# Kernel tuning notes

Hardware: AMD Instinct MI355X
Metric: run time of the kernel (lower is better)

The kernel has to match this reference:

```python
import jax, jax.numpy as jnp
import numpy as np

Q_MIN = 0.01
PT_THLD = 0.9
MAX_ETA = 4.0
LW_REP = 1.0
LW_NOISE = 0.1
LW_COWARD = 0.1
EPS = 1e-9

N_HITS = 50000
N_CLUSTERS = 1024  # cluster id 0 = noise, ids 1..K-1 = objects
D_EMB = 32


def setup_inputs() -> dict:
    key = jax.random.key(0)
    k0, k1, k2, k3, k4, k5 = jax.random.split(key, 6)
    beta = jax.random.uniform(k0, (N_HITS,), dtype=jnp.float32)
    x = jax.random.normal(k1, (N_HITS, D_EMB), dtype=jnp.float32)
    pt = jax.random.uniform(k2, (N_HITS,), dtype=jnp.float32)
    eta = jax.random.normal(k3, (N_HITS,), dtype=jnp.float32)
    reconstructable = jax.random.randint(k4, (N_HITS,), 0, 2, dtype=jnp.int32)
    cluster_ids = jax.random.randint(k5, (N_HITS,), 0, N_CLUSTERS, dtype=jnp.int64)
    return {
        'beta': beta, 'x': x, 'pt': pt, 'eta': eta,
        'reconstructable': reconstructable, 'cluster_ids': cluster_ids,
        'n_clusters': N_CLUSTERS,
    }


def reference(beta, x, pt, eta, reconstructable, cluster_ids, n_clusters):
    K = int(n_clusters)
    n_hits = beta.shape[0]
    n_part = K - 1  # objects of interest (excluding noise id 0)

    # charge q_j = arctanh(beta)^2 + q_min
    q = jnp.arctanh(jnp.clip(beta, 0.0, 1.0 - 1e-4)) ** 2 + Q_MIN  # [N]

    # attractive membership mask [N, K-1]: hit j belongs to object k and passes filters
    oids = jnp.arange(1, K)
    hit_ok = (reconstructable > 0) & (pt > PT_THLD) & (jnp.abs(eta) < MAX_ETA)
    att = (cluster_ids[:, None] == oids[None, :]) & hit_ok[:, None]
    attf = att.astype(q.dtype)

    # condensation point per object: hit with max charge within the object
    alphas = jnp.argmax(q[:, None] * attf, axis=0)  # [K-1]
    q_k = q[alphas]
    x_k = x[alphas]  # [K-1, D]

    # pairwise Euclidean distances, GEMM form (avoids [N,K,D] intermediate)
    d2 = (jnp.sum(x * x, axis=1)[:, None]
          + jnp.sum(x_k * x_k, axis=1)[None, :]
          - 2.0 * (x @ x_k.T))
    dist = jnp.sqrt(jnp.maximum(d2, 1e-12))  # [N, K-1]

    qw = q[:, None] * q_k[None, :]

    n_hits_oi = jnp.sum(hit_ok).astype(q.dtype)
    norm_att = EPS + n_hits_oi - n_part
    norm_rep = EPS + (n_part - 1) * n_hits

    v_att = jnp.sum(qw * (dist ** 2) * attf) / norm_att

    rep = (~att) & (dist < 1.0)  # max_n_rep=0 -> no subsampling
    v_rep = jnp.sum(qw * (1.0 - dist) * rep.astype(q.dtype)) / norm_rep

    l_coward = jnp.mean(1.0 - beta[alphas])

    noise_mask = (cluster_ids <= 0).astype(q.dtype)  # noise_threshold = 0
    l_noise = jnp.sum(beta * noise_mask) / jnp.maximum(jnp.sum(noise_mask), 1.0)

    total = v_att + LW_REP * v_rep + LW_NOISE * l_noise + LW_COWARD * l_coward
    return total
```

## Files before the change

kernel.cpp:

```cpp
#include <hip/hip_runtime.h>
#include <math.h>

namespace {

constexpr int D = 32;
constexpr int KOBJ = 1023;
constexpr float QMIN = 0.01f;
constexpr float PTT = 0.9f;
constexpr float METAETA = 4.0f;

typedef __attribute__((ext_vector_type(8))) short short8;
typedef __attribute__((ext_vector_type(4))) float f32x4;

__device__ inline float waveSum(float v) {
#pragma unroll
  for (int o = 32; o > 0; o >>= 1) v += __shfl_down(v, o, 64);
  return v;
}

__device__ inline ushort f2bf(float f) {
  unsigned u = __float_as_uint(f);
  return (ushort)((u + 0x7FFFu + ((u >> 16) & 1u)) >> 16);
}

__global__ void k_init(float* acc, int* flagNZ, unsigned long long* keys,
                       const int* __restrict__ cidw, int N) {
  int i = blockIdx.x * blockDim.x + threadIdx.x;
  if (i < KOBJ) keys[i] = 0ull;
  if (i < 8) acc[i] = 0.f;
  if (blockIdx.x == 0) {
    if (threadIdx.x == 0) flagNZ[0] = 0;
    __syncthreads();
    for (int jj = threadIdx.x; jj < 1024; jj += blockDim.x) {
      int idx = 2 * jj + 1;
      if (idx < N && cidw[idx] != 0) flagNZ[0] = 1;
    }
  }
}

__global__ __launch_bounds__(256) void k_hits(
    const float* __restrict__ beta, const float* __restrict__ x,
    const float* __restrict__ pt, const float* __restrict__ eta,
    const int* __restrict__ recon, const int* __restrict__ cidw,
    int N, const int* __restrict__ flagNZ,
    float* acc, unsigned long long* keys,
    float* __restrict__ qArr, float* __restrict__ nxArr,
    int* __restrict__ attkArr) {
  int t = threadIdx.x;
  int j = blockIdx.x * 256 + t;
  int is64 = (flagNZ[0] == 0);
  bool ok = false;
  if (j < N) {
    int cid = is64 ? cidw[2 * j] : cidw[j];
    float b = beta[j];
    float bc = fminf(fmaxf(b, 0.f), 1.f - 1e-4f);
    float tt = atanhf(bc);
    float q = tt * tt + QMIN;
    ok = (recon[j] > 0) && (pt[j] > PTT) && (fabsf(eta[j]) < METAETA);
    float nx = 0.f;
    const float4* xr = (const float4*)(x + (size_t)j * D);
#pragma unroll
    for (int i2 = 0; i2 < 8; ++i2) {
      float4 v = xr[i2];
      nx += v.x * v.x + v.y * v.y + v.z * v.z + v.w * v.w;
    }
    int attk = (ok && cid >= 1) ? cid : 0;
    qArr[j] = q;
    nxArr[j] = nx;
    attkArr[j] = attk;
    if (cid <= 0) {
      atomicAdd(&acc[2], b);
      atomicAdd(&acc[3], 1.f);
    }
    if (attk >= 1) {
      unsigned long long key =
          (((unsigned long long)__float_as_uint(q)) << 32) |
          (unsigned long long)(0xFFFFFFFFu - (unsigned)j);
      atomicMax(&keys[attk - 1], key);
    }
  }
  unsigned long long bal = __ballot(ok);
  if ((t & 63) == 0 && bal)
    atomicAdd(&acc[4], (float)__popcll(bal));
}

__global__ __launch_bounds__(256, 2) void k_clusters(
    const float* __restrict__ beta, const float* __restrict__ x,
    const unsigned long long* __restrict__ keys,
    const float* __restrict__ qArr, const float* __restrict__ nxArr,
    int* __restrict__ alphaArr, float2* __restrict__ qnk,
    ushort* __restrict__ xkbT, float* acc) {
  int k = blockIdx.x * blockDim.x + threadIdx.x;
  float cw = 0.f;
  if (k < KOBJ) {
    unsigned long long key = keys[k];
    int alpha = (key != 0ull) ? (int)(0xFFFFFFFFu - (unsigned)(key & 0xFFFFFFFFull)) : 0;
    alphaArr[k] = alpha;
    qnk[k] = make_float2(qArr[alpha], nxArr[alpha]);
    const float4* s4 = (const float4*)(x + (size_t)alpha * D);
    float4 v[8];
#pragma unroll
    for (int i = 0; i < 8; ++i) v[i] = s4[i];
#pragma unroll
    for (int s = 0; s < 4; ++s) {
      float4 v0 = v[2 * s], v1 = v[2 * s + 1];
      ushort* dst = xkbT + (size_t)s * 8192 + (size_t)k * 8;
      dst[0] = f2bf(v0.x); dst[1] = f2bf(v0.y);
      dst[2] = f2bf(v0.z); dst[3] = f2bf(v0.w);
      dst[4] = f2bf(v1.x); dst[5] = f2bf(v1.y);
      dst[6] = f2bf(v1.z); dst[7] = f2bf(v1.w);
    }
    cw = 1.f - beta[alpha];
  } else if (k == KOBJ) {
    qnk[k] = make_float2(0.f, 1e30f);
#pragma unroll
    for (int s = 0; s < 4; ++s) {
      ushort* dst = xkbT + (size_t)s * 8192 + (size_t)k * 8;
#pragma unroll
      for (int e = 0; e < 8; ++e) dst[e] = 0;
    }
  }
  float s = waveSum(cw);
  if ((threadIdx.x & 63) == 0 && s != 0.f) atomicAdd(&acc[5], s);
}

__global__ __launch_bounds__(256, 4) void k_pair(
    const float* __restrict__ x, int N,
    const float* __restrict__ qArr, const float* __restrict__ nxArr,
    const int* __restrict__ attkArr, const int* __restrict__ alphaArr,
    const float2* __restrict__ qnk, const ushort* __restrict__ xkbT,
    float* acc) {
  __shared__ char lds[16384 + 2048 + 48];
  float* redS = (float*)(lds + 16384 + 2048);
  int t = threadIdx.x;
  int wv = t >> 6;
  int ln = t & 63;
  int ot = blockIdx.y;
  int ob = ot * 256;
  int rowbase = blockIdx.x * 64;

#pragma unroll
  for (int i = 0; i < 4; ++i) {
    int c = wv * 4 + i;
    const char* src = (const char*)xkbT + (c >> 2) * 16384 + ob * 16 + (c & 3) * 1024;
    *(short8*)(lds + c * 1024 + ln * 16) = *(const short8*)(src + ln * 16);
  }
  if (wv < 2) {
    const char* src = (const char*)qnk + ob * 8 + wv * 1024;
    *(short8*)(lds + 16384 + wv * 1024 + ln * 16) = *(const short8*)(src + ln * 16);
  }

  int lr = ln & 15;
  int lk = ln >> 4;
  int wrow = rowbase + wv * 16;

  short8 am2;
  {
    int row = min(wrow + lr, N - 1);
    const float* p = x + (size_t)row * D + lk * 8;
    float4 v0 = *(const float4*)p;
    float4 v1 = *(const float4*)(p + 4);
    am2[0] = (short)f2bf(-2.f * v0.x); am2[1] = (short)f2bf(-2.f * v0.y);
    am2[2] = (short)f2bf(-2.f * v0.z); am2[3] = (short)f2bf(-2.f * v0.w);
    am2[4] = (short)f2bf(-2.f * v1.x); am2[5] = (short)f2bf(-2.f * v1.y);
    am2[6] = (short)f2bf(-2.f * v1.z); am2[7] = (short)f2bf(-2.f * v1.w);
  }
  float nxr[4], qrow[4];
#pragma unroll
  for (int i = 0; i < 4; ++i) {
    int row = wrow + lk * 4 + i;
    int rc = min(row, N - 1);
    nxr[i] = (row < N) ? nxArr[rc] : 1e37f;
    qrow[i] = (row < N) ? qArr[rc] : 0.f;
  }
  __syncthreads();

  const float2* qnkS = (const float2*)(lds + 16384);
  float rep = 0.f;
#pragma unroll
  for (int tt = 0; tt < 16; ++tt) {
    int o = tt * 16 + lr;
    short8 b = *(const short8*)(lds + lk * 4096 + o * 16);
    float2 qn = qnkS[o];
    float nk = qn.y;
    f32x4 c = {nxr[0] + nk, nxr[1] + nk, nxr[2] + nk, nxr[3] + nk};
    f32x4 s = __builtin_amdgcn_mfma_f32_16x16x32_bf16(am2, b, c, 0, 0, 0);
    float m = fminf(fminf(s[0], s[1]), fminf(s[2], s[3]));
    if (__any(m < 1.f)) {
      float qk = qn.x;
#pragma unroll
      for (int i = 0; i < 4; ++i) {
        if (s[i] < 1.f)
          rep += qrow[i] * qk * (1.f - sqrtf(fmaxf(s[i], 1e-12f)));
      }
    }
  }

  float attc = 0.f, repSub = 0.f;
  if (ot == 0) {
    int j = rowbase + (t >> 2);
    int qt = t & 3;
    if (j < N) {
      int attk = attkArr[j];
      if (attk >= 1) {
        int k0 = attk - 1;
        int alpha = alphaArr[k0];
        float2 qn = qnk[k0];
        const float4* xj = (const float4*)(x + (size_t)j * D + qt * 8);
        const float4* xk = (const float4*)(x + (size_t)alpha * D + qt * 8);
        float4 a0 = xj[0], a1 = xj[1], b0 = xk[0], b1 = xk[1];
        float dot = a0.x * b0.x + a0.y * b0.y + a0.z * b0.z + a0.w * b0.w
                  + a1.x * b1.x + a1.y * b1.y + a1.z * b1.z + a1.w * b1.w;
        dot += __shfl_xor(dot, 1, 4);
        dot += __shfl_xor(dot, 2, 4);
        if (qt == 0) {
          float d2 = nxArr[j] + qn.y - 2.f * dot;
          float w = qArr[j] * qn.x;
          attc = w * fmaxf(d2, 1e-12f);
          if (d2 < 1.f)
            repSub = w * (1.f - sqrtf(fmaxf(d2, 1e-12f)));
        }
      }
    }
  }

  float sw = waveSum(rep);
  float sa = waveSum(attc);
  float sr = waveSum(repSub);
  if (ln == 0) {
    redS[wv] = sw;
    redS[4 + wv] = sa;
    redS[8 + wv] = sr;
  }
  __syncthreads();
  if (t == 0) {
    float tot = (redS[0] + redS[1]) + (redS[2] + redS[3]);
    float ta = (redS[4] + redS[5]) + (redS[6] + redS[7]);
    float tr = (redS[8] + redS[9]) + (redS[10] + redS[11]);
    if (tot != tr) atomicAdd(&acc[1], tot - tr);
    if (ta != 0.f) atomicAdd(&acc[0], ta);
  }
}

__global__ void k_final(const float* __restrict__ acc, int N, float* out) {
  if (threadIdx.x == 0 && blockIdx.x == 0) {
    double attSum = acc[0], repSum = acc[1], noiseSum = acc[2];
    double noiseCnt = acc[3], okCnt = acc[4], cowardSum = acc[5];
    double norm_att = 1e-9 + okCnt - (double)KOBJ;
    double norm_rep = 1e-9 + (double)(KOBJ - 1) * (double)N;
    double v_att = attSum / norm_att;
    double v_rep = repSum / norm_rep;
    double l_coward = cowardSum / (double)KOBJ;
    double l_noise = noiseSum / fmax(noiseCnt, 1.0);
    out[0] = (float)(v_att + 1.0 * v_rep + 0.1 * l_noise + 0.1 * l_coward);
  }
}

}

extern "C" void kernel_launch(void* const* d_in, const int* in_sizes, int n_in,
                              void* d_out, int out_size, void* d_ws, size_t ws_size,
                              hipStream_t stream) {
  const float* beta = (const float*)d_in[0];
  const float* x = (const float*)d_in[1];
  const float* pt = (const float*)d_in[2];
  const float* eta = (const float*)d_in[3];
  const int* recon = (const int*)d_in[4];
  const int* cidw = (const int*)d_in[5];
  int N = in_sizes[0];
  float* out = (float*)d_out;

  char* w = (char*)d_ws;
  float* acc = (float*)w;
  int* flagNZ = (int*)(w + 40);
  unsigned long long* keys = (unsigned long long*)(w + 64);
  int* alphaArr = (int*)(w + 8256);
  float2* qnk = (float2*)(w + 12352);
  ushort* xkbT = (ushort*)(w + 20544);
  float* qArr = (float*)(w + 86080);
  float* nxArr = (float*)(w + 86080 + (size_t)N * 4);
  int* attkArr = (int*)(w + 86080 + (size_t)N * 8);

  int nbN = (N + 255) / 256;
  int rowgroups = (N + 63) / 64;

  k_init<<<4, 256, 0, stream>>>(acc, flagNZ, keys, cidw, N);
  k_hits<<<nbN, 256, 0, stream>>>(beta, x, pt, eta, recon, cidw, N, flagNZ,
                                  acc, keys, qArr, nxArr, attkArr);
  k_clusters<<<4, 256, 0, stream>>>(beta, x, keys, qArr, nxArr,
                                    alphaArr, qnk, xkbT, acc);
  dim3 gp(rowgroups, 4);
  k_pair<<<gp, 256, 0, stream>>>(x, N, qArr, nxArr, attkArr,
                                 alphaArr, qnk, xkbT, acc);
  k_final<<<1, 64, 0, stream>>>(acc, N, out);
}
```

Measured before the change: 62.69 us.

## Process two row tiles per wave, load object tile via global_load_lds, branchless repulsion

Each block now covers 128 rows instead of 64. Every wave issues two MFMAs per object tile, so each LDS-staged object tile is reused across twice as many hit rows and half as many blocks restage it. The object tile and charges are copied straight into LDS with global_load_lds instead of going through registers. The __any-guarded repulsion branch becomes a branchless fmaxf(0, 1-sqrt) form, which evaluates sqrt for every pair and trades compute for no divergence; the main loop's unroll is reduced to 4 and the occupancy hint is dropped.

```diff
diff --git a/kernel.cpp b/kernel.cpp
--- a/kernel.cpp
+++ b/kernel.cpp
@@ -11,6 +11,11 @@
 
 typedef __attribute__((ext_vector_type(8))) short short8;
 typedef __attribute__((ext_vector_type(4))) float f32x4;
+
+#define GLOAD_LDS16(g, l)                                              \
+  __builtin_amdgcn_global_load_lds(                                    \
+      (const __attribute__((address_space(1))) void*)(g),              \
+      (__attribute__((address_space(3))) void*)(l), 16, 0, 0)
 
 __device__ inline float waveSum(float v) {
 #pragma unroll
@@ -124,95 +129,99 @@
   if ((threadIdx.x & 63) == 0 && s != 0.f) atomicAdd(&acc[5], s);
 }
 
-__global__ __launch_bounds__(256, 4) void k_pair(
+__global__ __launch_bounds__(256) void k_pair(
     const float* __restrict__ x, int N,
     const float* __restrict__ qArr, const float* __restrict__ nxArr,
     const int* __restrict__ attkArr, const int* __restrict__ alphaArr,
     const float2* __restrict__ qnk, const ushort* __restrict__ xkbT,
     float* acc) {
-  __shared__ char lds[16384 + 2048 + 48];
-  float* redS = (float*)(lds + 16384 + 2048);
+  __shared__ char lds[16384 + 2048 + 64];
+  float* redS = (float*)(lds + 18432);
   int t = threadIdx.x;
   int wv = t >> 6;
   int ln = t & 63;
   int ot = blockIdx.y;
   int ob = ot * 256;
-  int rowbase = blockIdx.x * 64;
-
-#pragma unroll
-  for (int i = 0; i < 4; ++i) {
-    int c = wv * 4 + i;
-    const char* src = (const char*)xkbT + (c >> 2) * 16384 + ob * 16 + (c & 3) * 1024;
-    *(short8*)(lds + c * 1024 + ln * 16) = *(const short8*)(src + ln * 16);
-  }
-  if (wv < 2) {
-    const char* src = (const char*)qnk + ob * 8 + wv * 1024;
-    *(short8*)(lds + 16384 + wv * 1024 + ln * 16) = *(const short8*)(src + ln * 16);
+  int rowbase = blockIdx.x * 128;
+
+  for (int c = wv; c < 18; c += 4) {
+    const char* src;
+    if (c < 16)
+      src = (const char*)xkbT + (c >> 2) * 16384 + ob * 16 + (c & 3) * 1024;
+    else
+      src = (const char*)qnk + ob * 8 + (c - 16) * 1024;
+    GLOAD_LDS16(src + ln * 16, lds + c * 1024);
   }
 
   int lr = ln & 15;
   int lk = ln >> 4;
-  int wrow = rowbase + wv * 16;
-
-  short8 am2;
-  {
-    int row = min(wrow + lr, N - 1);
+  int wrow = rowbase + wv * 32;
+
+  short8 am2[2];
+#pragma unroll
+  for (int rt = 0; rt < 2; ++rt) {
+    int row = min(wrow + rt * 16 + lr, N - 1);
     const float* p = x + (size_t)row * D + lk * 8;
     float4 v0 = *(const float4*)p;
     float4 v1 = *(const float4*)(p + 4);
-    am2[0] = (short)f2bf(-2.f * v0.x); am2[1] = (short)f2bf(-2.f * v0.y);
-    am2[2] = (short)f2bf(-2.f * v0.z); am2[3] = (short)f2bf(-2.f * v0.w);
-    am2[4] = (short)f2bf(-2.f * v1.x); am2[5] = (short)f2bf(-2.f * v1.y);
-    am2[6] = (short)f2bf(-2.f * v1.z); am2[7] = (short)f2bf(-2.f * v1.w);
-  }
-  float nxr[4], qrow[4];
-#pragma unroll
-  for (int i = 0; i < 4; ++i) {
-    int row = wrow + lk * 4 + i;
-    int rc = min(row, N - 1);
-    nxr[i] = (row < N) ? nxArr[rc] : 1e37f;
-    qrow[i] = (row < N) ? qArr[rc] : 0.f;
-  }
+    short8 a;
+    a[0] = (short)f2bf(-2.f * v0.x); a[1] = (short)f2bf(-2.f * v0.y);
+    a[2] = (short)f2bf(-2.f * v0.z); a[3] = (short)f2bf(-2.f * v0.w);
+    a[4] = (short)f2bf(-2.f * v1.x); a[5] = (short)f2bf(-2.f * v1.y);
+    a[6] = (short)f2bf(-2.f * v1.z); a[7] = (short)f2bf(-2.f * v1.w);
+    am2[rt] = a;
+  }
+  float nxr[2][4], qrow[2][4];
+#pragma unroll
+  for (int rt = 0; rt < 2; ++rt)
+#pragma unroll
+    for (int i = 0; i < 4; ++i) {
+      int row = wrow + rt * 16 + lk * 4 + i;
+      int rc = min(row, N - 1);
+      nxr[rt][i] = (row < N) ? nxArr[rc] : 1e37f;
+      qrow[rt][i] = (row < N) ? qArr[rc] : 0.f;
+    }
   __syncthreads();
 
   const float2* qnkS = (const float2*)(lds + 16384);
   float rep = 0.f;
-#pragma unroll
+#pragma unroll 4
   for (int tt = 0; tt < 16; ++tt) {
     int o = tt * 16 + lr;
     short8 b = *(const short8*)(lds + lk * 4096 + o * 16);
     float2 qn = qnkS[o];
     float nk = qn.y;
-    f32x4 c = {nxr[0] + nk, nxr[1] + nk, nxr[2] + nk, nxr[3] + nk};
-    f32x4 s = __builtin_amdgcn_mfma_f32_16x16x32_bf16(am2, b, c, 0, 0, 0);
-    float m = fminf(fminf(s[0], s[1]), fminf(s[2], s[3]));
-    if (__any(m < 1.f)) {
-      float qk = qn.x;
-#pragma unroll
-      for (int i = 0; i < 4; ++i) {
-        if (s[i] < 1.f)
-          rep += qrow[i] * qk * (1.f - sqrtf(fmaxf(s[i], 1e-12f)));
-      }
+    float qk = qn.x;
+    f32x4 c0 = {nxr[0][0] + nk, nxr[0][1] + nk, nxr[0][2] + nk, nxr[0][3] + nk};
+    f32x4 c1 = {nxr[1][0] + nk, nxr[1][1] + nk, nxr[1][2] + nk, nxr[1][3] + nk};
+    f32x4 s0 = __builtin_amdgcn_mfma_f32_16x16x32_bf16(am2[0], b, c0, 0, 0, 0);
+    f32x4 s1 = __builtin_amdgcn_mfma_f32_16x16x32_bf16(am2[1], b, c1, 0, 0, 0);
+#pragma unroll
+    for (int i = 0; i < 4; ++i) {
+      rep += qrow[0][i] * qk * fmaxf(0.f, 1.f - sqrtf(fmaxf(s0[i], 1e-12f)));
+      rep += qrow[1][i] * qk * fmaxf(0.f, 1.f - sqrtf(fmaxf(s1[i], 1e-12f)));
     }
   }
 
   float attc = 0.f, repSub = 0.f;
   if (ot == 0) {
-    int j = rowbase + (t >> 2);
-    int qt = t & 3;
+    int j = rowbase + (t >> 1);
+    int qt = t & 1;
     if (j < N) {
       int attk = attkArr[j];
       if (attk >= 1) {
         int k0 = attk - 1;
         int alpha = alphaArr[k0];
         float2 qn = qnk[k0];
-        const float4* xj = (const float4*)(x + (size_t)j * D + qt * 8);
-        const float4* xk = (const float4*)(x + (size_t)alpha * D + qt * 8);
-        float4 a0 = xj[0], a1 = xj[1], b0 = xk[0], b1 = xk[1];
-        float dot = a0.x * b0.x + a0.y * b0.y + a0.z * b0.z + a0.w * b0.w
-                  + a1.x * b1.x + a1.y * b1.y + a1.z * b1.z + a1.w * b1.w;
-        dot += __shfl_xor(dot, 1, 4);
-        dot += __shfl_xor(dot, 2, 4);
+        const float4* xj = (const float4*)(x + (size_t)j * D + qt * 16);
+        const float4* xk = (const float4*)(x + (size_t)alpha * D + qt * 16);
+        float dot = 0.f;
+#pragma unroll
+        for (int i = 0; i < 4; ++i) {
+          float4 a = xj[i], bb = xk[i];
+          dot += a.x * bb.x + a.y * bb.y + a.z * bb.z + a.w * bb.w;
+        }
+        dot += __shfl_xor(dot, 1, 2);
         if (qt == 0) {
           float d2 = nxArr[j] + qn.y - 2.f * dot;
           float w = qArr[j] * qn.x;
@@ -282,7 +291,7 @@
   int* attkArr = (int*)(w + 86080 + (size_t)N * 8);
 
   int nbN = (N + 255) / 256;
-  int rowgroups = (N + 63) / 64;
+  int rowgroups = (N + 127) / 128;
 
   k_init<<<4, 256, 0, stream>>>(acc, flagNZ, keys, cidw, N);
   k_hits<<<nbN, 256, 0, stream>>>(beta, x, pt, eta, recon, cidw, N, flagNZ,
```

Result: slower. 68.63 us (+9.5%).
